# Optimization experiments

Measured on AMD Instinct MI355X. Metric: run time of the kernel, lower is better.

Reference implementation:

```python
import jax, jax.numpy as jnp
import numpy as np

B, S, D, H = 4, 2048, 1024, 16
DK = D // H
INFTY = 1000000.0
INIT_SCALE = 1.2  # RandomUniform(-1.2, 1.2) kernel initializer


def setup_inputs() -> dict:
    key = jax.random.key(0)
    ks = jax.random.split(key, 6)
    x = jax.random.normal(ks[0], (B, S, D), dtype=jnp.float32)
    mask = jax.random.randint(ks[1], (B, S), 0, 2) == 1  # bool padding mask
    WQ = jax.random.uniform(ks[2], (D, D), jnp.float32, -INIT_SCALE, INIT_SCALE)
    WK = jax.random.uniform(ks[3], (D, D), jnp.float32, -INIT_SCALE, INIT_SCALE)
    WV = jax.random.uniform(ks[4], (D, D), jnp.float32, -INIT_SCALE, INIT_SCALE)
    WO = jax.random.uniform(ks[5], (D, D), jnp.float32, -INIT_SCALE, INIT_SCALE)
    return {"x": x, "mask": mask, "WQ": WQ, "WK": WK, "WV": WV, "WO": WO}


def reference(x, mask, WQ, WK, WV, WO):
    # Faithful reproduction of the layout: reshape to (B, S, d_key, n_heads)
    # then permute, matching K.reshape/K.permute_dimensions in the original.
    q = (x @ WQ).reshape(B, S, DK, H).transpose(0, 3, 1, 2)  # (B, H, S, DK)
    k = (x @ WK).reshape(B, S, DK, H).transpose(0, 3, 2, 1)  # (B, H, DK, S)
    score = jnp.matmul(q, k) / np.sqrt(DK)                   # (B, H, S, S)
    # additive key masking: score - (~mask)[B,1,1,S] * infinity
    inv_mask = (~mask).astype(x.dtype)
    score = score - inv_mask[:, None, None, :] * INFTY
    score = jax.nn.softmax(score, axis=-1)                   # att_dropout == 0
    v = (x @ WV).reshape(B, S, DK, H).transpose(0, 3, 1, 2)  # (B, H, S, DK)
    o = jnp.matmul(score, v)                                 # (B, H, S, DK)
    o = o.transpose(0, 2, 1, 3).reshape(B, S, H * DK)
    o = o @ WO                                               # (B, S, D)
    # final query-position masking + abs, as in the original
    o = jnp.abs(o * mask.astype(x.dtype)[:, :, None])
    return o
```

## Files before the change

### kernel.cpp

```cpp
#include <hip/hip_runtime.h>
#include <hip/hip_bf16.h>
#include <cstdint>
#include <cstddef>

constexpr int Bc  = 4;
constexpr int Sc  = 2048;
constexpr int Dc  = 1024;
constexpr int Hc  = 16;
constexpr int DKc = 64;
constexpr int Mtot = Bc * Sc;
constexpr float SC2  = 0.125f * 1.4426950408889634f;
constexpr float INF2 = 1000000.0f * 1.4426950408889634f;
constexpr float SXq  = 5400.0f;
constexpr float SWq  = 27166.0f;
constexpr float INVS = 1.0f / (SXq * SWq);

typedef short bf16x8 __attribute__((ext_vector_type(8)));
typedef float f32x4  __attribute__((ext_vector_type(4)));
typedef int   i32x4  __attribute__((ext_vector_type(4)));
typedef unsigned int u32x4 __attribute__((ext_vector_type(4)));

__device__ inline unsigned short bf16_rn(float f) {
    uint32_t u = __float_as_uint(f);
    uint32_t r = (u + 0x7FFFu + ((u >> 16) & 1u)) >> 16;
    return (unsigned short)r;
}
__device__ inline uint32_t pk_bf16(float a, float b) {
    uint32_t d;
    asm("v_cvt_pk_bf16_f32 %0, %1, %2" : "=v"(d) : "v"(a), "v"(b));
    return d;
}
__device__ inline int perm64(int k) {
    return (k & ~63) | (((k & 15) << 2) | ((k >> 4) & 3));
}
__device__ inline void mfma_i8(i32x4& acc, u32x4 a, u32x4 b) {
    asm volatile("v_mfma_i32_16x16x64_i8 %0, %1, %2, %0" : "+v"(acc) : "v"(a), "v"(b));
}
__device__ inline void split_i16(int fx, char& h, char& l) {
    int lo = ((fx + 128) & 255) - 128;
    h = (char)((fx - lo) >> 8);
    l = (char)lo;
}
__device__ inline void gl_lds16(const void* g, void* l) {
    __builtin_amdgcn_global_load_lds(
        (const __attribute__((address_space(1))) unsigned int*)g,
        (__attribute__((address_space(3))) unsigned int*)l, 16, 0, 0);
}

__global__ __launch_bounds__(256) void mask_norm(const void* __restrict__ mraw,
                                                 int* __restrict__ mi,
                                                 int* __restrict__ rinv,
                                                 int* __restrict__ nbv,
                                                 int* __restrict__ npadv) {
    __shared__ int fF32, fU8, fI32;
    __shared__ int part[256];
    __shared__ int nb_sh;
    if (threadIdx.x == 0) { fF32 = 0; fU8 = 0; fI32 = 0; }
    __syncthreads();
    const unsigned char* mb = (const unsigned char*)mraw;
    int aF = 0, a1 = 0, a4 = 0;
    for (int i = threadIdx.x; i < Mtot; i += 256) {
        unsigned char v = mb[i];
        if ((i & 3) == 3 && v == 0x3F) aF = 1;
        if (v) {
            if (i & 3) a1 = 1;
            else if (i & 7) a4 = 1;
        }
    }
    if (aF) fF32 = 1;
    if (a1) fU8 = 1;
    if (a4) fI32 = 1;
    __syncthreads();
    if (fF32) {
        const float* mf = (const float*)mraw;
        for (int s = threadIdx.x; s < Mtot; s += 256) mi[s] = (mf[s] != 0.0f);
    } else if (fU8) {
        for (int s = threadIdx.x; s < Mtot; s += 256) mi[s] = (mb[s] != 0);
    } else if (fI32) {
        const int* m32 = (const int*)mraw;
        for (int s = threadIdx.x; s < Mtot; s += 256) mi[s] = (m32[s] != 0);
    } else {
        const long long* m64 = (const long long*)mraw;
        for (int s = threadIdx.x; s < Mtot; s += 256) mi[s] = (m64[s] != 0);
    }
    __syncthreads();

    for (int b = 0; b < Bc; ++b) {
        const int* mrow = mi + b * Sc;
        int loc[8], cnt = 0;
        #pragma unroll
        for (int u = 0; u < 8; ++u) {
            loc[u] = mrow[threadIdx.x * 8 + u];
            cnt += loc[u];
        }
        part[threadIdx.x] = cnt;
        __syncthreads();
        if (threadIdx.x == 0) {
            int run = 0;
            for (int i = 0; i < 256; ++i) { int c = part[i]; part[i] = run; run += c; }
            nbv[b] = run;
            npadv[b] = (run + 63) & ~63;
            nb_sh = run;
        }
        __syncthreads();
        const int nbb = nb_sh;
        int pos = part[threadIdx.x];
        #pragma unroll
        for (int u = 0; u < 8; ++u) {
            const int s = threadIdx.x * 8 + u;
            if (loc[u]) {
                rinv[b * Sc + pos] = s;
                pos++;
            } else {
                rinv[b * Sc + nbb + (s - pos)] = s;
            }
        }
        __syncthreads();
    }
}

__global__ __launch_bounds__(256) void zero_pad(const int* __restrict__ nbv,
                                                const int* __restrict__ npadv,
                                                unsigned short* __restrict__ Khi,
                                                unsigned short* __restrict__ Klo,
                                                unsigned short* __restrict__ Vt) {
    const int bh = blockIdx.x;
    const int b = bh >> 4;
    const int nb = nbv[b], np = npadv[b];
    const int t = threadIdx.x;
    const size_t kbase = (size_t)bh * Sc * DKc;
    const size_t vbase = (size_t)bh * DKc * Sc;
    const int n = (np - nb) * DKc;
    for (int i = t; i < n; i += 256) {
        const int r = nb + i / DKc, c = i % DKc;
        Khi[kbase + (size_t)r * DKc + c] = 0;
        Klo[kbase + (size_t)r * DKc + c] = 0;
        Vt[vbase + (size_t)c * Sc + r] = 0;
    }
}

__global__ __launch_bounds__(256) void quant_x(const float* __restrict__ x,
                                               unsigned short* __restrict__ xhi,
                                               signed char* __restrict__ xh8,
                                               signed char* __restrict__ xl8) {
    const int i = (blockIdx.x * 256 + threadIdx.x) * 4;
    float4 v = *reinterpret_cast<const float4*>(x + i);
    ushort4 hb;
    hb.x = bf16_rn(v.x); hb.y = bf16_rn(v.y); hb.z = bf16_rn(v.z); hb.w = bf16_rn(v.w);
    *reinterpret_cast<ushort4*>(xhi + i) = hb;
    char4 h8, l8;
    int fx;
    fx = min(max(__float2int_rn(v.x * SXq), -32640), 32640); split_i16(fx, h8.x, l8.x);
    fx = min(max(__float2int_rn(v.y * SXq), -32640), 32640); split_i16(fx, h8.y, l8.y);
    fx = min(max(__float2int_rn(v.z * SXq), -32640), 32640); split_i16(fx, h8.z, l8.z);
    fx = min(max(__float2int_rn(v.w * SXq), -32640), 32640); split_i16(fx, h8.w, l8.w);
    *reinterpret_cast<char4*>(xh8 + i) = h8;
    *reinterpret_cast<char4*>(xl8 + i) = l8;
}

template<bool PERM>
__global__ __launch_bounds__(256) void split_wt(const float* __restrict__ W,
                                                unsigned short* __restrict__ WhT) {
    __shared__ float ls[64][68];
    const int k0 = blockIdx.y * 64, n0 = blockIdx.x * 64;
    const int t = threadIdx.x;
    #pragma unroll
    for (int l = 0; l < 4; ++l) {
        const int idx = t + l * 256;
        const int r = idx >> 4, c = (idx & 15) * 4;
        *reinterpret_cast<float4*>(&ls[r][c]) =
            *reinterpret_cast<const float4*>(W + (size_t)(k0 + r) * Dc + n0 + c);
    }
    __syncthreads();
    #pragma unroll
    for (int l = 0; l < 4; ++l) {
        const int idx = t + l * 256;
        const int on = idx >> 4, kq = (idx & 15) * 4;
        #pragma unroll
        for (int j = 0; j < 4; ++j) {
            const float v = ls[kq + j][on];
            const int k  = k0 + kq + j;
            const int kd = PERM ? perm64(k) : k;
            WhT[(size_t)(n0 + on) * Dc + kd] = bf16_rn(v);
        }
    }
}

__global__ __launch_bounds__(256) void split_wt_i8(const float* __restrict__ W,
                                                   signed char* __restrict__ Wh8,
                                                   signed char* __restrict__ Wl8) {
    __shared__ float ls[64][68];
    const int k0 = blockIdx.y * 64, n0 = blockIdx.x * 64;
    const int t = threadIdx.x;
    #pragma unroll
    for (int l = 0; l < 4; ++l) {
        const int idx = t + l * 256;
        const int r = idx >> 4, c = (idx & 15) * 4;
        *reinterpret_cast<float4*>(&ls[r][c]) =
            *reinterpret_cast<const float4*>(W + (size_t)(k0 + r) * Dc + n0 + c);
    }
    __syncthreads();
    #pragma unroll
    for (int l = 0; l < 4; ++l) {
        const int idx = t + l * 256;
        const int on = idx >> 4, kq = (idx & 15) * 4;
        char4 hv, lv;
        int fx;
        fx = __float2int_rn(ls[kq + 0][on] * SWq); split_i16(fx, hv.x, lv.x);
        fx = __float2int_rn(ls[kq + 1][on] * SWq); split_i16(fx, hv.y, lv.y);
        fx = __float2int_rn(ls[kq + 2][on] * SWq); split_i16(fx, hv.z, lv.z);
        fx = __float2int_rn(ls[kq + 3][on] * SWq); split_i16(fx, hv.w, lv.w);
        const size_t o = (size_t)(n0 + on) * Dc + k0 + kq;
        *reinterpret_cast<char4*>(Wh8 + o) = hv;
        *reinterpret_cast<char4*>(Wl8 + o) = lv;
    }
}

__global__ __launch_bounds__(256) void gemm_i8qk(
    const signed char* __restrict__ Ah8, const signed char* __restrict__ Al8,
    const signed char* __restrict__ Bh8, const signed char* __restrict__ Bl8,
    const int* __restrict__ rinv, const int* __restrict__ nbv, float scale,
    unsigned short* __restrict__ O1, unsigned short* __restrict__ O2) {
    __shared__ __align__(16) signed char Ah[128 * 64];
    __shared__ __align__(16) signed char Al[128 * 64];
    __shared__ __align__(16) signed char Bh[128 * 64];
    __shared__ __align__(16) signed char Bl[128 * 64];
    const int t = threadIdx.x;
    const int n0 = blockIdx.x * 128, m0 = blockIdx.y * 128;
    const int b = m0 >> 11, mm0 = m0 & 2047;
    const int nb = nbv[b];
    if (mm0 >= nb) return;
    const int wv = t >> 6, lane = t & 63, li = lane & 15, lg = lane >> 4;
    const int wm = (wv >> 1) * 64, wn = (wv & 1) * 64;

    size_t gAr[2];
    int rowN[2];
    #pragma unroll
    for (int c = 0; c < 2; ++c) {
        const int ci  = wv * 2 + c;
        const int row = ci * 16 + (lane >> 2);
        rowN[c] = n0 + row;
        gAr[c] = ((size_t)b * Sc + rinv[b * Sc + mm0 + row]) * Dc;
    }
    const int cq = (lane & 3) * 16;

    i32x4 a1[4][4] = {};
    i32x4 a2[4][4] = {};
    asm volatile("s_nop 7" :::);

    for (int k0 = 0; k0 < Dc; k0 += 64) {
        __syncthreads();
        #pragma unroll
        for (int c = 0; c < 2; ++c) {
            const int ci = wv * 2 + c;
            const size_t ga = gAr[c] + k0 + cq;
            const size_t gb = (size_t)rowN[c] * Dc + k0 + cq;
            gl_lds16(Ah8 + ga, &Ah[ci * 1024]);
            gl_lds16(Al8 + ga, &Al[ci * 1024]);
            gl_lds16(Bh8 + gb, &Bh[ci * 1024]);
            gl_lds16(Bl8 + gb, &Bl[ci * 1024]);
        }
        __syncthreads();

        u32x4 bhf[4], blf[4];
        #pragma unroll
        for (int ni = 0; ni < 4; ++ni) {
            bhf[ni] = *reinterpret_cast<const u32x4*>(&Bh[(wn + ni * 16 + li) * 64 + lg * 16]);
            blf[ni] = *reinterpret_cast<const u32x4*>(&Bl[(wn + ni * 16 + li) * 64 + lg * 16]);
        }
        #pragma unroll
        for (int mi = 0; mi < 4; ++mi) {
            const u32x4 ahf = *reinterpret_cast<const u32x4*>(&Ah[(wm + mi * 16 + li) * 64 + lg * 16]);
            const u32x4 alf = *reinterpret_cast<const u32x4*>(&Al[(wm + mi * 16 + li) * 64 + lg * 16]);
            #pragma unroll
            for (int ni = 0; ni < 4; ++ni) {
                mfma_i8(a1[mi][ni], ahf, bhf[ni]);
                mfma_i8(a2[mi][ni], ahf, blf[ni]);
                mfma_i8(a2[mi][ni], alf, bhf[ni]);
            }
        }
    }

    asm volatile("s_nop 7\ns_nop 7\ns_nop 7" :::);

    const int dkb = (n0 + wn) >> 4;
    #pragma unroll
    for (int mi = 0; mi < 4; ++mi) {
        #pragma unroll
        for (int r = 0; r < 4; ++r) {
            const int cs = mm0 + wm + mi * 16 + lg * 4 + r;
            if (cs >= nb) continue;
            const size_t ob = ((size_t)(b * Hc + li) * Sc + cs) * DKc + dkb;
            ushort4 hq, lq;
            float fv[4];
            #pragma unroll
            for (int ni = 0; ni < 4; ++ni)
                fv[ni] = fmaf((float)a1[mi][ni][r], 65536.0f,
                              (float)a2[mi][ni][r] * 256.0f) * scale;
            hq.x = bf16_rn(fv[0]); hq.y = bf16_rn(fv[1]);
            hq.z = bf16_rn(fv[2]); hq.w = bf16_rn(fv[3]);
            lq.x = bf16_rn(fv[0] - __uint_as_float((uint32_t)hq.x << 16));
            lq.y = bf16_rn(fv[1] - __uint_as_float((uint32_t)hq.y << 16));
            lq.z = bf16_rn(fv[2] - __uint_as_float((uint32_t)hq.z << 16));
            lq.w = bf16_rn(fv[3] - __uint_as_float((uint32_t)hq.w << 16));
            *reinterpret_cast<ushort4*>(O1 + ob) = hq;
            *reinterpret_cast<ushort4*>(O2 + ob) = lq;
        }
    }
}

template<int EPI>
__global__ __launch_bounds__(256) void gemm_bf16(
    const unsigned short* __restrict__ Ahi,
    const unsigned short* __restrict__ Bhi,
    const int* __restrict__ rinv, const int* __restrict__ nbv,
    unsigned short* __restrict__ O1,
    float* __restrict__ Of) {
    __shared__ __align__(16) unsigned short Ah[128 * 32];
    __shared__ __align__(16) unsigned short Bh[128 * 32];
    const int t = threadIdx.x;
    const int n0 = blockIdx.x * 128, m0 = blockIdx.y * 128;
    const int b = m0 >> 11, mm0 = m0 & 2047;
    const int nb = nbv[b];
    const int wv = t >> 6, lane = t & 63, li = lane & 15, lg = lane >> 4;
    const int wm = (wv >> 1) * 64, wn = (wv & 1) * 64;

    if (EPI == 1 && mm0 >= nb) return;
    if (EPI == 2 && mm0 >= nb) {
        #pragma unroll
        for (int mi = 0; mi < 4; ++mi) {
            #pragma unroll
            for (int r = 0; r < 4; ++r) {
                const int cs = mm0 + wm + mi * 16 + lg * 4 + r;
                const int gs = rinv[b * Sc + cs];
                #pragma unroll
                for (int ni = 0; ni < 4; ++ni) {
                    const int n = n0 + wn + ni * 16 + li;
                    Of[((size_t)(b * Sc + gs)) * Dc + n] = 0.0f;
                }
            }
        }
        return;
    }

    size_t gAr[2];
    int rowN[2];
    #pragma unroll
    for (int c = 0; c < 2; ++c) {
        const int ci  = wv * 2 + c;
        const int row = ci * 16 + (lane >> 2);
        rowN[c] = n0 + row;
        if (EPI == 1)
            gAr[c] = ((size_t)b * Sc + rinv[b * Sc + mm0 + row]) * Dc;
        else
            gAr[c] = (size_t)(m0 + row) * Dc;
    }
    const int cq = (lane & 3) * 8;

    f32x4 acc[4][4] = {};

    for (int k0 = 0; k0 < Dc; k0 += 32) {
        __syncthreads();
        #pragma unroll
        for (int c = 0; c < 2; ++c) {
            const int ci = wv * 2 + c;
            gl_lds16(Ahi + gAr[c] + k0 + cq, &Ah[ci * 512]);
            gl_lds16(Bhi + (size_t)rowN[c] * Dc + k0 + cq, &Bh[ci * 512]);
        }
        __syncthreads();

        bf16x8 bhf[4];
        #pragma unroll
        for (int ni = 0; ni < 4; ++ni)
            bhf[ni] = *reinterpret_cast<const bf16x8*>(&Bh[(wn + ni * 16 + li) * 32 + lg * 8]);
        #pragma unroll
        for (int mi = 0; mi < 4; ++mi) {
            const bf16x8 ahf = *reinterpret_cast<const bf16x8*>(&Ah[(wm + mi * 16 + li) * 32 + lg * 8]);
            #pragma unroll
            for (int ni = 0; ni < 4; ++ni)
                acc[mi][ni] = __builtin_amdgcn_mfma_f32_16x16x32_bf16(ahf, bhf[ni], acc[mi][ni], 0, 0, 0);
        }
    }

    #pragma unroll
    for (int mi = 0; mi < 4; ++mi) {
        if (EPI == 1) {
            const int csb = mm0 + wm + mi * 16 + lg * 4;
            #pragma unroll
            for (int ni = 0; ni < 4; ++ni) {
                const int n = n0 + wn + ni * 16 + li;
                const int h = n & 15, dk = n >> 4;
                const size_t ob = ((size_t)(b * Hc + h) * DKc + dk) * Sc + csb;
                if (csb + 3 < nb) {
                    ushort4 vq;
                    vq.x = bf16_rn(acc[mi][ni][0]);
                    vq.y = bf16_rn(acc[mi][ni][1]);
                    vq.z = bf16_rn(acc[mi][ni][2]);
                    vq.w = bf16_rn(acc[mi][ni][3]);
                    *reinterpret_cast<ushort4*>(O1 + ob) = vq;
                } else {
                    #pragma unroll
                    for (int r = 0; r < 4; ++r)
                        if (csb + r < nb) O1[ob + r] = bf16_rn(acc[mi][ni][r]);
                }
            }
        } else {
            #pragma unroll
            for (int r = 0; r < 4; ++r) {
                const int cs = mm0 + wm + mi * 16 + lg * 4 + r;
                const int gs = rinv[b * Sc + cs];
                const bool valid = (cs < nb);
                #pragma unroll
                for (int ni = 0; ni < 4; ++ni) {
                    const int n = n0 + wn + ni * 16 + li;
                    Of[((size_t)(b * Sc + gs)) * Dc + n] =
                        valid ? fabsf(acc[mi][ni][r]) : 0.0f;
                }
            }
        }
    }
}

__global__ __launch_bounds__(512) void attn_mfma(const unsigned short* __restrict__ Qhi,
                                                 const unsigned short* __restrict__ Qlo,
                                                 const unsigned short* __restrict__ Khi,
                                                 const unsigned short* __restrict__ Klo,
                                                 const unsigned short* __restrict__ Vtg,
                                                 const int* __restrict__ nbv,
                                                 const int* __restrict__ npadv,
                                                 unsigned short* __restrict__ att) {
    constexpr int TK = 64;
    const int id  = blockIdx.x;
    const int swz = (id & 7) * 128 + (id >> 3);
    const int qb  = swz & 15;
    const int bh  = swz >> 4;
    const int b = bh >> 4, h = bh & 15;
    const int q0 = qb * 128;
    const int nb = nbv[b];
    if (q0 >= nb) return;
    const int ntile = npadv[b] >> 6;
    const int nt2 = (ntile + 1) >> 1;

    __shared__ __align__(16) unsigned short PsKs[2][128][72];
    __shared__ __align__(16) unsigned short Vs[2][80][72];

    const int t    = threadIdx.x;
    const int grp  = t >> 8;
    const int tg   = t & 255;
    const int wave = tg >> 6;
    const int lane = t & 63;
    const int lg   = lane >> 4;
    const int li   = lane & 15;

    const int myBase = grp ? nt2 : 0;
    const int myEnd  = grp ? ntile : nt2;

    {
        const int r = 64 + (tg >> 4), c4 = (tg & 15) * 4;
        const unsigned short val = ((tg >> 4) == 0) ? (unsigned short)0x3F80 : (unsigned short)0;
        ushort4 v; v.x = val; v.y = val; v.z = val; v.w = val;
        *reinterpret_cast<ushort4*>(&Vs[grp][r][c4]) = v;
    }

    bf16x8 qh[2][2], ql[2][2];
    #pragma unroll
    for (int hf = 0; hf < 2; ++hf) {
        const size_t qrow = ((size_t)bh * Sc + q0 + wave * 32 + hf * 16 + li) * DKc + lg * 8;
        qh[hf][0] = *reinterpret_cast<const bf16x8*>(Qhi + qrow);
        qh[hf][1] = *reinterpret_cast<const bf16x8*>(Qhi + qrow + 32);
        ql[hf][0] = *reinterpret_cast<const bf16x8*>(Qlo + qrow);
        ql[hf][1] = *reinterpret_cast<const bf16x8*>(Qlo + qrow + 32);
    }

    const size_t kbase = (size_t)bh * Sc * DKc;
    const size_t vbase = (size_t)bh * DKc * Sc;

    f32x4 accO[2][5] = {};
    float m[2][4];
    #pragma unroll
    for (int hf = 0; hf < 2; ++hf)
        #pragma unroll
        for (int r = 0; r < 4; ++r) m[hf][r] = -1e30f;

    for (int it = 0; it < nt2; ++it) {
        const int kt = myBase + it;
        const bool act = (kt < myEnd);
        const int k0 = kt * TK;
        __syncthreads();
        if (act) {
            #pragma unroll
            for (int u = 0; u < 2; ++u) {
                const int idx = tg + u * 256;
                const int r = idx >> 3, cc = (idx & 7) * 8;
                *reinterpret_cast<uint4*>(&PsKs[grp][r][cc]) =
                    *reinterpret_cast<const uint4*>(Khi + kbase + (size_t)(k0 + r) * DKc + cc);
                *reinterpret_cast<uint4*>(&PsKs[grp][64 + r][cc]) =
                    *reinterpret_cast<const uint4*>(Klo + kbase + (size_t)(k0 + r) * DKc + cc);
                *reinterpret_cast<uint4*>(&Vs[grp][r][cc]) =
                    *reinterpret_cast<const uint4*>(Vtg + vbase + (size_t)r * Sc + k0 + cc);
            }
        }
        __syncthreads();
        if (!act) continue;

        float sc[2][4][4];
        #pragma unroll
        for (int n = 0; n < 4; ++n) {
            const bf16x8 kh0 = *reinterpret_cast<const bf16x8*>(&PsKs[grp][n * 16 + li][lg * 8]);
            const bf16x8 kh1 = *reinterpret_cast<const bf16x8*>(&PsKs[grp][n * 16 + li][32 + lg * 8]);
            const bf16x8 kl0 = *reinterpret_cast<const bf16x8*>(&PsKs[grp][64 + n * 16 + li][lg * 8]);
            const bf16x8 kl1 = *reinterpret_cast<const bf16x8*>(&PsKs[grp][64 + n * 16 + li][32 + lg * 8]);
            const float mz = (k0 + n * 16 + li < nb) ? 0.0f : INF2;
            #pragma unroll
            for (int hf = 0; hf < 2; ++hf) {
                f32x4 a = {0, 0, 0, 0};
                a = __builtin_amdgcn_mfma_f32_16x16x32_bf16(qh[hf][0], kh0, a, 0, 0, 0);
                a = __builtin_amdgcn_mfma_f32_16x16x32_bf16(qh[hf][1], kh1, a, 0, 0, 0);
                a = __builtin_amdgcn_mfma_f32_16x16x32_bf16(qh[hf][0], kl0, a, 0, 0, 0);
                a = __builtin_amdgcn_mfma_f32_16x16x32_bf16(qh[hf][1], kl1, a, 0, 0, 0);
                a = __builtin_amdgcn_mfma_f32_16x16x32_bf16(ql[hf][0], kh0, a, 0, 0, 0);
                a = __builtin_amdgcn_mfma_f32_16x16x32_bf16(ql[hf][1], kh1, a, 0, 0, 0);
                #pragma unroll
                for (int r = 0; r < 4; ++r) sc[hf][n][r] = a[r] - mz;
            }
        }

        float mx[2][4], rs[2][4];
        #pragma unroll
        for (int hf = 0; hf < 2; ++hf)
            #pragma unroll
            for (int r = 0; r < 4; ++r)
                mx[hf][r] = fmaxf(fmaxf(sc[hf][0][r], sc[hf][1][r]),
                                  fmaxf(sc[hf][2][r], sc[hf][3][r]));
        #pragma unroll
        for (int o = 1; o < 16; o <<= 1)
            #pragma unroll
            for (int hf = 0; hf < 2; ++hf)
                #pragma unroll
                for (int r = 0; r < 4; ++r)
                    mx[hf][r] = fmaxf(mx[hf][r], __shfl_xor(mx[hf][r], o));
        #pragma unroll
        for (int hf = 0; hf < 2; ++hf)
            #pragma unroll
            for (int r = 0; r < 4; ++r) {
                const float mn = fmaxf(m[hf][r], mx[hf][r]);
                rs[hf][r] = exp2f(m[hf][r] - mn);
                m[hf][r]  = mn;
            }
        #pragma unroll
        for (int hf = 0; hf < 2; ++hf)
            #pragma unroll
            for (int r = 0; r < 4; ++r) {
                const int row = wave * 32 + hf * 16 + lg * 4 + r;
                const uint32_t w01 = pk_bf16(exp2f(sc[hf][0][r] - m[hf][r]),
                                             exp2f(sc[hf][1][r] - m[hf][r]));
                const uint32_t w23 = pk_bf16(exp2f(sc[hf][2][r] - m[hf][r]),
                                             exp2f(sc[hf][3][r] - m[hf][r]));
                PsKs[grp][row][li]      = (unsigned short)w01;
                PsKs[grp][row][li + 16] = (unsigned short)(w01 >> 16);
                PsKs[grp][row][li + 32] = (unsigned short)w23;
                PsKs[grp][row][li + 48] = (unsigned short)(w23 >> 16);
            }

        #pragma unroll
        for (int hf = 0; hf < 2; ++hf)
            #pragma unroll
            for (int dt = 0; dt < 5; ++dt)
                #pragma unroll
                for (int r = 0; r < 4; ++r)
                    accO[hf][dt][r] *= rs[hf][r];

        #pragma unroll
        for (int c = 0; c < 2; ++c) {
            bf16x8 pa[2];
            #pragma unroll
            for (int hf = 0; hf < 2; ++hf)
                pa[hf] = *reinterpret_cast<const bf16x8*>(&PsKs[grp][wave * 32 + hf * 16 + li][c * 32 + lg * 8]);
            #pragma unroll
            for (int dt = 0; dt < 5; ++dt) {
                const bf16x8 vb = *reinterpret_cast<const bf16x8*>(&Vs[grp][dt * 16 + li][c * 32 + lg * 8]);
                #pragma unroll
                for (int hf = 0; hf < 2; ++hf)
                    accO[hf][dt] = __builtin_amdgcn_mfma_f32_16x16x32_bf16(pa[hf], vb, accO[hf][dt], 0, 0, 0);
            }
        }
    }

    __syncthreads();
    float* pO  = (float*)&PsKs[0][0][0];
    float* pML = pO + 128 * 64;

    if (grp == 1) {
        #pragma unroll
        for (int hf = 0; hf < 2; ++hf) {
            #pragma unroll
            for (int r = 0; r < 4; ++r) {
                const int row = wave * 32 + hf * 16 + lg * 4 + r;
                if (li == 0) {
                    pML[row * 2]     = m[hf][r];
                    pML[row * 2 + 1] = accO[hf][4][r];
                }
                float4 o = make_float4(accO[hf][0][r], accO[hf][1][r],
                                       accO[hf][2][r], accO[hf][3][r]);
                *reinterpret_cast<float4*>(&pO[row * 64 + li * 4]) = o;
            }
        }
    }
    __syncthreads();
    if (grp == 0) {
        #pragma unroll
        for (int hf = 0; hf < 2; ++hf) {
            #pragma unroll
            for (int r = 0; r < 4; ++r) {
                const int row = wave * 32 + hf * 16 + lg * 4 + r;
                const float m1 = pML[row * 2];
                const float l1 = pML[row * 2 + 1];
                const float l0 = __shfl(accO[hf][4][r], lane & 0x30);
                const float ms = fmaxf(m[hf][r], m1);
                const float s0 = exp2f(m[hf][r] - ms);
                const float s1 = exp2f(m1 - ms);
                const float inv = 1.0f / (l0 * s0 + l1 * s1);
                const float4 o1 = *reinterpret_cast<const float4*>(&pO[row * 64 + li * 4]);
                const int q = q0 + row;
                uint2 w;
                w.x = pk_bf16((accO[hf][0][r] * s0 + o1.x * s1) * inv,
                              (accO[hf][1][r] * s0 + o1.y * s1) * inv);
                w.y = pk_bf16((accO[hf][2][r] * s0 + o1.z * s1) * inv,
                              (accO[hf][3][r] * s0 + o1.w * s1) * inv);
                *reinterpret_cast<uint2*>(att + (size_t)(b * Sc + q) * Dc + h * DKc + li * 4) = w;
            }
        }
    }
}

extern "C" void kernel_launch(void* const* d_in, const int* in_sizes, int n_in,
                              void* d_out, int out_size, void* d_ws, size_t ws_size,
                              hipStream_t stream) {
    const float* x    = (const float*)d_in[0];
    const void*  mraw = d_in[1];
    const float* WQ   = (const float*)d_in[2];
    const float* WK   = (const float*)d_in[3];
    const float* WV   = (const float*)d_in[4];
    const float* WO   = (const float*)d_in[5];
    float* out = (float*)d_out;

    int* mi    = (int*)d_ws;
    int* rinv  = mi + Mtot;
    int* nbv   = rinv + Mtot;
    int* npadv = nbv + 4;
    const size_t SZ = (size_t)Mtot * Dc;
    const size_t WSZ = (size_t)Dc * Dc;
    char* p = (char*)d_ws + 65664;
    unsigned short* xhi = (unsigned short*)p;            p += SZ * 2;
    signed char*    xh8 = (signed char*)p;               p += SZ;
    signed char*    xl8 = (signed char*)p;               p += SZ;
    unsigned short* WVh = (unsigned short*)p;            p += WSZ * 2;
    unsigned short* WOh = (unsigned short*)p;            p += WSZ * 2;
    signed char*    WQh8 = (signed char*)p;              p += WSZ;
    signed char*    WQl8 = (signed char*)p;              p += WSZ;
    signed char*    WKh8 = (signed char*)p;              p += WSZ;
    signed char*    WKl8 = (signed char*)p;              p += WSZ;
    unsigned short* Qhi = (unsigned short*)p;            p += SZ * 2;
    unsigned short* Qlo = (unsigned short*)p;            p += SZ * 2;
    unsigned short* Khi = (unsigned short*)p;            p += SZ * 2;
    unsigned short* Klo = (unsigned short*)p;            p += SZ * 2;
    unsigned short* Vt  = (unsigned short*)p;            p += SZ * 2;
    unsigned short* att = xhi;

    mask_norm<<<1, 256, 0, stream>>>(mraw, mi, rinv, nbv, npadv);
    quant_x<<<(int)(SZ / 1024), 256, 0, stream>>>(x, xhi, xh8, xl8);
    const dim3 gW(16, 16);
    split_wt_i8<<<gW, 256, 0, stream>>>(WQ, WQh8, WQl8);
    split_wt_i8<<<gW, 256, 0, stream>>>(WK, WKh8, WKl8);
    split_wt<false><<<gW, 256, 0, stream>>>(WV, WVh);
    split_wt<true ><<<gW, 256, 0, stream>>>(WO, WOh);
    zero_pad<<<dim3(64), 256, 0, stream>>>(nbv, npadv, Khi, Klo, Vt);

    const dim3 gG(Dc / 128, Mtot / 128);
    gemm_i8qk<<<gG, 256, 0, stream>>>(xh8, xl8, WQh8, WQl8, rinv, nbv, SC2 * INVS, Qhi, Qlo);
    gemm_i8qk<<<gG, 256, 0, stream>>>(xh8, xl8, WKh8, WKl8, rinv, nbv, INVS, Khi, Klo);
    gemm_bf16<1><<<gG, 256, 0, stream>>>(xhi, WVh, rinv, nbv, Vt, nullptr);

    attn_mfma<<<dim3(1024), 512, 0, stream>>>(Qhi, Qlo, Khi, Klo, Vt, nbv, npadv, att);

    gemm_bf16<2><<<gG, 256, 0, stream>>>(att, WOh, rinv, nbv, nullptr, out);
}
```

Baseline: 298.8 us.

## Merge prep kernels and QKV GEMMs into batched launches, parallelize mask per batch

```diff
diff --git a/kernel.cpp b/kernel.cpp
--- a/kernel.cpp
+++ b/kernel.cpp
@@ -48,7 +48,6 @@
 }
 
 __global__ __launch_bounds__(256) void mask_norm(const void* __restrict__ mraw,
-                                                 int* __restrict__ mi,
                                                  int* __restrict__ rinv,
                                                  int* __restrict__ nbv,
                                                  int* __restrict__ npadv) {
@@ -71,71 +70,47 @@
     if (a1) fU8 = 1;
     if (a4) fI32 = 1;
     __syncthreads();
+
+    const int b = blockIdx.x;
+    const int sbase = b * Sc + threadIdx.x * 8;
+    int loc[8], cnt = 0;
     if (fF32) {
         const float* mf = (const float*)mraw;
-        for (int s = threadIdx.x; s < Mtot; s += 256) mi[s] = (mf[s] != 0.0f);
+        #pragma unroll
+        for (int u = 0; u < 8; ++u) { loc[u] = (mf[sbase + u] != 0.0f); cnt += loc[u]; }
     } else if (fU8) {
-        for (int s = threadIdx.x; s < Mtot; s += 256) mi[s] = (mb[s] != 0);
+        #pragma unroll
+        for (int u = 0; u < 8; ++u) { loc[u] = (mb[sbase + u] != 0); cnt += loc[u]; }
     } else if (fI32) {
         const int* m32 = (const int*)mraw;
-        for (int s = threadIdx.x; s < Mtot; s += 256) mi[s] = (m32[s] != 0);
+        #pragma unroll
+        for (int u = 0; u < 8; ++u) { loc[u] = (m32[sbase + u] != 0); cnt += loc[u]; }
     } else {
         const long long* m64 = (const long long*)mraw;
-        for (int s = threadIdx.x; s < Mtot; s += 256) mi[s] = (m64[s] != 0);
-    }
+        #pragma unroll
+        for (int u = 0; u < 8; ++u) { loc[u] = (m64[sbase + u] != 0); cnt += loc[u]; }
+    }
+    part[threadIdx.x] = cnt;
     __syncthreads();
-
-    for (int b = 0; b < Bc; ++b) {
-        const int* mrow = mi + b * Sc;
-        int loc[8], cnt = 0;
-        #pragma unroll
-        for (int u = 0; u < 8; ++u) {
-            loc[u] = mrow[threadIdx.x * 8 + u];
-            cnt += loc[u];
-        }
-        part[threadIdx.x] = cnt;
-        __syncthreads();
-        if (threadIdx.x == 0) {
-            int run = 0;
-            for (int i = 0; i < 256; ++i) { int c = part[i]; part[i] = run; run += c; }
-            nbv[b] = run;
-            npadv[b] = (run + 63) & ~63;
-            nb_sh = run;
-        }
-        __syncthreads();
-        const int nbb = nb_sh;
-        int pos = part[threadIdx.x];
-        #pragma unroll
-        for (int u = 0; u < 8; ++u) {
-            const int s = threadIdx.x * 8 + u;
-            if (loc[u]) {
-                rinv[b * Sc + pos] = s;
-                pos++;
-            } else {
-                rinv[b * Sc + nbb + (s - pos)] = s;
-            }
-        }
-        __syncthreads();
-    }
-}
-
-__global__ __launch_bounds__(256) void zero_pad(const int* __restrict__ nbv,
-                                                const int* __restrict__ npadv,
-                                                unsigned short* __restrict__ Khi,
-                                                unsigned short* __restrict__ Klo,
-                                                unsigned short* __restrict__ Vt) {
-    const int bh = blockIdx.x;
-    const int b = bh >> 4;
-    const int nb = nbv[b], np = npadv[b];
-    const int t = threadIdx.x;
-    const size_t kbase = (size_t)bh * Sc * DKc;
-    const size_t vbase = (size_t)bh * DKc * Sc;
-    const int n = (np - nb) * DKc;
-    for (int i = t; i < n; i += 256) {
-        const int r = nb + i / DKc, c = i % DKc;
-        Khi[kbase + (size_t)r * DKc + c] = 0;
-        Klo[kbase + (size_t)r * DKc + c] = 0;
-        Vt[vbase + (size_t)c * Sc + r] = 0;
+    if (threadIdx.x == 0) {
+        int run = 0;
+        for (int i = 0; i < 256; ++i) { int c = part[i]; part[i] = run; run += c; }
+        nbv[b] = run;
+        npadv[b] = (run + 63) & ~63;
+        nb_sh = run;
+    }
+    __syncthreads();
+    const int nbb = nb_sh;
+    int pos = part[threadIdx.x];
+    #pragma unroll
+    for (int u = 0; u < 8; ++u) {
+        const int s = threadIdx.x * 8 + u;
+        if (loc[u]) {
+            rinv[b * Sc + pos] = s;
+            pos++;
+        } else {
+            rinv[b * Sc + nbb + (s - pos)] = s;
+        }
     }
 }
 
@@ -158,12 +133,38 @@
     *reinterpret_cast<char4*>(xl8 + i) = l8;
 }
 
-template<bool PERM>
-__global__ __launch_bounds__(256) void split_wt(const float* __restrict__ W,
-                                                unsigned short* __restrict__ WhT) {
+__global__ __launch_bounds__(256) void prep_w(
+    const float* __restrict__ WQ, const float* __restrict__ WK,
+    const float* __restrict__ WV, const float* __restrict__ WO,
+    signed char* __restrict__ WQh8, signed char* __restrict__ WQl8,
+    signed char* __restrict__ WKh8, signed char* __restrict__ WKl8,
+    unsigned short* __restrict__ WVh, unsigned short* __restrict__ WOh,
+    const int* __restrict__ nbv, const int* __restrict__ npadv,
+    unsigned short* __restrict__ Khi, unsigned short* __restrict__ Klo,
+    unsigned short* __restrict__ Vt) {
+    const int z = blockIdx.z;
+    const int t = threadIdx.x;
+
+    if (z == 4) {
+        const int idx = blockIdx.y * 16 + blockIdx.x;
+        const int bh = idx >> 2, prt = idx & 3;
+        const int b = bh >> 4;
+        const int nb = nbv[b], np = npadv[b];
+        const size_t kbase = (size_t)bh * Sc * DKc;
+        const size_t vbase = (size_t)bh * DKc * Sc;
+        const int n = (np - nb) * DKc;
+        for (int i = prt * 256 + t; i < n; i += 1024) {
+            const int r = nb + i / DKc, c = i % DKc;
+            Khi[kbase + (size_t)r * DKc + c] = 0;
+            Klo[kbase + (size_t)r * DKc + c] = 0;
+            Vt[vbase + (size_t)c * Sc + r] = 0;
+        }
+        return;
+    }
+
     __shared__ float ls[64][68];
+    const float* W = (z == 0) ? WQ : (z == 1) ? WK : (z == 2) ? WV : WO;
     const int k0 = blockIdx.y * 64, n0 = blockIdx.x * 64;
-    const int t = threadIdx.x;
     #pragma unroll
     for (int l = 0; l < 4; ++l) {
         const int idx = t + l * 256;
@@ -172,59 +173,54 @@
             *reinterpret_cast<const float4*>(W + (size_t)(k0 + r) * Dc + n0 + c);
     }
     __syncthreads();
-    #pragma unroll
-    for (int l = 0; l < 4; ++l) {
-        const int idx = t + l * 256;
-        const int on = idx >> 4, kq = (idx & 15) * 4;
-        #pragma unroll
-        for (int j = 0; j < 4; ++j) {
-            const float v = ls[kq + j][on];
-            const int k  = k0 + kq + j;
-            const int kd = PERM ? perm64(k) : k;
-            WhT[(size_t)(n0 + on) * Dc + kd] = bf16_rn(v);
-        }
-    }
-}
-
-__global__ __launch_bounds__(256) void split_wt_i8(const float* __restrict__ W,
-                                                   signed char* __restrict__ Wh8,
-                                                   signed char* __restrict__ Wl8) {
-    __shared__ float ls[64][68];
-    const int k0 = blockIdx.y * 64, n0 = blockIdx.x * 64;
-    const int t = threadIdx.x;
-    #pragma unroll
-    for (int l = 0; l < 4; ++l) {
-        const int idx = t + l * 256;
-        const int r = idx >> 4, c = (idx & 15) * 4;
-        *reinterpret_cast<float4*>(&ls[r][c]) =
-            *reinterpret_cast<const float4*>(W + (size_t)(k0 + r) * Dc + n0 + c);
-    }
-    __syncthreads();
-    #pragma unroll
-    for (int l = 0; l < 4; ++l) {
-        const int idx = t + l * 256;
-        const int on = idx >> 4, kq = (idx & 15) * 4;
-        char4 hv, lv;
-        int fx;
-        fx = __float2int_rn(ls[kq + 0][on] * SWq); split_i16(fx, hv.x, lv.x);
-        fx = __float2int_rn(ls[kq + 1][on] * SWq); split_i16(fx, hv.y, lv.y);
-        fx = __float2int_rn(ls[kq + 2][on] * SWq); split_i16(fx, hv.z, lv.z);
-        fx = __float2int_rn(ls[kq + 3][on] * SWq); split_i16(fx, hv.w, lv.w);
-        const size_t o = (size_t)(n0 + on) * Dc + k0 + kq;
-        *reinterpret_cast<char4*>(Wh8 + o) = hv;
-        *reinterpret_cast<char4*>(Wl8 + o) = lv;
-    }
-}
-
-__global__ __launch_bounds__(256) void gemm_i8qk(
-    const signed char* __restrict__ Ah8, const signed char* __restrict__ Al8,
-    const signed char* __restrict__ Bh8, const signed char* __restrict__ Bl8,
-    const int* __restrict__ rinv, const int* __restrict__ nbv, float scale,
-    unsigned short* __restrict__ O1, unsigned short* __restrict__ O2) {
-    __shared__ __align__(16) signed char Ah[128 * 64];
-    __shared__ __align__(16) signed char Al[128 * 64];
-    __shared__ __align__(16) signed char Bh[128 * 64];
-    __shared__ __align__(16) signed char Bl[128 * 64];
+
+    if (z <= 1) {
+        signed char* Wh8 = z ? WKh8 : WQh8;
+        signed char* Wl8 = z ? WKl8 : WQl8;
+        #pragma unroll
+        for (int l = 0; l < 4; ++l) {
+            const int idx = t + l * 256;
+            const int on = idx >> 4, kq = (idx & 15) * 4;
+            char4 hv, lv;
+            int fx;
+            fx = __float2int_rn(ls[kq + 0][on] * SWq); split_i16(fx, hv.x, lv.x);
+            fx = __float2int_rn(ls[kq + 1][on] * SWq); split_i16(fx, hv.y, lv.y);
+            fx = __float2int_rn(ls[kq + 2][on] * SWq); split_i16(fx, hv.z, lv.z);
+            fx = __float2int_rn(ls[kq + 3][on] * SWq); split_i16(fx, hv.w, lv.w);
+            const size_t o = (size_t)(n0 + on) * Dc + k0 + kq;
+            *reinterpret_cast<char4*>(Wh8 + o) = hv;
+            *reinterpret_cast<char4*>(Wl8 + o) = lv;
+        }
+    } else {
+        unsigned short* Wh = (z == 2) ? WVh : WOh;
+        const bool PERM = (z == 3);
+        #pragma unroll
+        for (int l = 0; l < 4; ++l) {
+            const int idx = t + l * 256;
+            const int on = idx >> 4, kq = (idx & 15) * 4;
+            #pragma unroll
+            for (int j = 0; j < 4; ++j) {
+                const float v = ls[kq + j][on];
+                const int k  = k0 + kq + j;
+                const int kd = PERM ? perm64(k) : k;
+                Wh[(size_t)(n0 + on) * Dc + kd] = bf16_rn(v);
+            }
+        }
+    }
+}
+
+__global__ __launch_bounds__(256) void gemm_qkv(
+    const signed char* __restrict__ xh8, const signed char* __restrict__ xl8,
+    const unsigned short* __restrict__ xhi,
+    const signed char* __restrict__ WQh8, const signed char* __restrict__ WQl8,
+    const signed char* __restrict__ WKh8, const signed char* __restrict__ WKl8,
+    const unsigned short* __restrict__ WVh,
+    const int* __restrict__ rinv, const int* __restrict__ nbv,
+    unsigned short* __restrict__ Qhi, unsigned short* __restrict__ Qlo,
+    unsigned short* __restrict__ Khi, unsigned short* __restrict__ Klo,
+    unsigned short* __restrict__ Vt) {
+    __shared__ __align__(16) char S[32768];
+    const int z = blockIdx.z;
     const int t = threadIdx.x;
     const int n0 = blockIdx.x * 128, m0 = blockIdx.y * 128;
     const int b = m0 >> 11, mm0 = m0 & 2047;
@@ -233,158 +229,133 @@
     const int wv = t >> 6, lane = t & 63, li = lane & 15, lg = lane >> 4;
     const int wm = (wv >> 1) * 64, wn = (wv & 1) * 64;
 
-    size_t gAr[2];
-    int rowN[2];
-    #pragma unroll
-    for (int c = 0; c < 2; ++c) {
-        const int ci  = wv * 2 + c;
-        const int row = ci * 16 + (lane >> 2);
-        rowN[c] = n0 + row;
-        gAr[c] = ((size_t)b * Sc + rinv[b * Sc + mm0 + row]) * Dc;
-    }
-    const int cq = (lane & 3) * 16;
-
-    i32x4 a1[4][4] = {};
-    i32x4 a2[4][4] = {};
-    asm volatile("s_nop 7" :::);
-
-    for (int k0 = 0; k0 < Dc; k0 += 64) {
-        __syncthreads();
+    if (z < 2) {
+        signed char* Ah = (signed char*)S;
+        signed char* Al = (signed char*)S + 8192;
+        signed char* Bh = (signed char*)S + 16384;
+        signed char* Bl = (signed char*)S + 24576;
+        const signed char* Bh8 = z ? WKh8 : WQh8;
+        const signed char* Bl8 = z ? WKl8 : WQl8;
+        const float scale = z ? INVS : (SC2 * INVS);
+        unsigned short* O1 = z ? Khi : Qhi;
+        unsigned short* O2 = z ? Klo : Qlo;
+
+        size_t gAr[2];
+        int rowN[2];
         #pragma unroll
         for (int c = 0; c < 2; ++c) {
-            const int ci = wv * 2 + c;
-            const size_t ga = gAr[c] + k0 + cq;
-            const size_t gb = (size_t)rowN[c] * Dc + k0 + cq;
-            gl_lds16(Ah8 + ga, &Ah[ci * 1024]);
-            gl_lds16(Al8 + ga, &Al[ci * 1024]);
-            gl_lds16(Bh8 + gb, &Bh[ci * 1024]);
-            gl_lds16(Bl8 + gb, &Bl[ci * 1024]);
-        }
-        __syncthreads();
-
-        u32x4 bhf[4], blf[4];
-        #pragma unroll
-        for (int ni = 0; ni < 4; ++ni) {
-            bhf[ni] = *reinterpret_cast<const u32x4*>(&Bh[(wn + ni * 16 + li) * 64 + lg * 16]);
-            blf[ni] = *reinterpret_cast<const u32x4*>(&Bl[(wn + ni * 16 + li) * 64 + lg * 16]);
-        }
-        #pragma unroll
-        for (int mi = 0; mi < 4; ++mi) {
-            const u32x4 ahf = *reinterpret_cast<const u32x4*>(&Ah[(wm + mi * 16 + li) * 64 + lg * 16]);
-            const u32x4 alf = *reinterpret_cast<const u32x4*>(&Al[(wm + mi * 16 + li) * 64 + lg * 16]);
+            const int ci  = wv * 2 + c;
+            const int row = ci * 16 + (lane >> 2);
+            rowN[c] = n0 + row;
+            gAr[c] = ((size_t)b * Sc + rinv[b * Sc + mm0 + row]) * Dc;
+        }
+        const int cq = (lane & 3) * 16;
+
+        i32x4 a1[4][4] = {};
+        i32x4 a2[4][4] = {};
+        asm volatile("s_nop 7" :::);
+
+        for (int k0 = 0; k0 < Dc; k0 += 64) {
+            __syncthreads();
+            #pragma unroll
+            for (int c = 0; c < 2; ++c) {
+                const int ci = wv * 2 + c;
+                const size_t ga = gAr[c] + k0 + cq;
+                const size_t gb = (size_t)rowN[c] * Dc + k0 + cq;
+                gl_lds16(xh8 + ga, &Ah[ci * 1024]);
+                gl_lds16(xl8 + ga, &Al[ci * 1024]);
+                gl_lds16(Bh8 + gb, &Bh[ci * 1024]);
+                gl_lds16(Bl8 + gb, &Bl[ci * 1024]);
+            }
+            __syncthreads();
+
+            u32x4 bhf[4], blf[4];
             #pragma unroll
             for (int ni = 0; ni < 4; ++ni) {
-                mfma_i8(a1[mi][ni], ahf, bhf[ni]);
-                mfma_i8(a2[mi][ni], ahf, blf[ni]);
-                mfma_i8(a2[mi][ni], alf, bhf[ni]);
-            }
-        }
-    }
-
-    asm volatile("s_nop 7\ns_nop 7\ns_nop 7" :::);
-
-    const int dkb = (n0 + wn) >> 4;
-    #pragma unroll
-    for (int mi = 0; mi < 4; ++mi) {
-        #pragma unroll
-        for (int r = 0; r < 4; ++r) {
-            const int cs = mm0 + wm + mi * 16 + lg * 4 + r;
-            if (cs >= nb) continue;
-            const size_t ob = ((size_t)(b * Hc + li) * Sc + cs) * DKc + dkb;
-            ushort4 hq, lq;
-            float fv[4];
-            #pragma unroll
-            for (int ni = 0; ni < 4; ++ni)
-                fv[ni] = fmaf((float)a1[mi][ni][r], 65536.0f,
-                              (float)a2[mi][ni][r] * 256.0f) * scale;
-            hq.x = bf16_rn(fv[0]); hq.y = bf16_rn(fv[1]);
-            hq.z = bf16_rn(fv[2]); hq.w = bf16_rn(fv[3]);
-            lq.x = bf16_rn(fv[0] - __uint_as_float((uint32_t)hq.x << 16));
-            lq.y = bf16_rn(fv[1] - __uint_as_float((uint32_t)hq.y << 16));
-            lq.z = bf16_rn(fv[2] - __uint_as_float((uint32_t)hq.z << 16));
-            lq.w = bf16_rn(fv[3] - __uint_as_float((uint32_t)hq.w << 16));
-            *reinterpret_cast<ushort4*>(O1 + ob) = hq;
-            *reinterpret_cast<ushort4*>(O2 + ob) = lq;
-        }
-    }
-}
-
-template<int EPI>
-__global__ __launch_bounds__(256) void gemm_bf16(
-    const unsigned short* __restrict__ Ahi,
-    const unsigned short* __restrict__ Bhi,
-    const int* __restrict__ rinv, const int* __restrict__ nbv,
-    unsigned short* __restrict__ O1,
-    float* __restrict__ Of) {
-    __shared__ __align__(16) unsigned short Ah[128 * 32];
-    __shared__ __align__(16) unsigned short Bh[128 * 32];
-    const int t = threadIdx.x;
-    const int n0 = blockIdx.x * 128, m0 = blockIdx.y * 128;
-    const int b = m0 >> 11, mm0 = m0 & 2047;
-    const int nb = nbv[b];
-    const int wv = t >> 6, lane = t & 63, li = lane & 15, lg = lane >> 4;
-    const int wm = (wv >> 1) * 64, wn = (wv & 1) * 64;
-
-    if (EPI == 1 && mm0 >= nb) return;
-    if (EPI == 2 && mm0 >= nb) {
+                bhf[ni] = *reinterpret_cast<const u32x4*>(&Bh[(wn + ni * 16 + li) * 64 + lg * 16]);
+                blf[ni] = *reinterpret_cast<const u32x4*>(&Bl[(wn + ni * 16 + li) * 64 + lg * 16]);
+            }
+            #pragma unroll
+            for (int mi = 0; mi < 4; ++mi) {
+                const u32x4 ahf = *reinterpret_cast<const u32x4*>(&Ah[(wm + mi * 16 + li) * 64 + lg * 16]);
+                const u32x4 alf = *reinterpret_cast<const u32x4*>(&Al[(wm + mi * 16 + li) * 64 + lg * 16]);
+                #pragma unroll
+                for (int ni = 0; ni < 4; ++ni) {
+                    mfma_i8(a1[mi][ni], ahf, bhf[ni]);
+                    mfma_i8(a2[mi][ni], ahf, blf[ni]);
+                    mfma_i8(a2[mi][ni], alf, bhf[ni]);
+                }
+            }
+        }
+
+        asm volatile("s_nop 7\ns_nop 7\ns_nop 7" :::);
+
+        const int dkb = (n0 + wn) >> 4;
         #pragma unroll
         for (int mi = 0; mi < 4; ++mi) {
             #pragma unroll
             for (int r = 0; r < 4; ++r) {
                 const int cs = mm0 + wm + mi * 16 + lg * 4 + r;
-                const int gs = rinv[b * Sc + cs];
+                if (cs >= nb) continue;
+                const size_t ob = ((size_t)(b * Hc + li) * Sc + cs) * DKc + dkb;
+                ushort4 hq, lq;
+                float fv[4];
                 #pragma unroll
-                for (int ni = 0; ni < 4; ++ni) {
-                    const int n = n0 + wn + ni * 16 + li;
-                    Of[((size_t)(b * Sc + gs)) * Dc + n] = 0.0f;
-                }
-            }
-        }
-        return;
-    }
-
-    size_t gAr[2];
-    int rowN[2];
-    #pragma unroll
-    for (int c = 0; c < 2; ++c) {
-        const int ci  = wv * 2 + c;
-        const int row = ci * 16 + (lane >> 2);
-        rowN[c] = n0 + row;
-        if (EPI == 1)
+                for (int ni = 0; ni < 4; ++ni)
+                    fv[ni] = fmaf((float)a1[mi][ni][r], 65536.0f,
+                                  (float)a2[mi][ni][r] * 256.0f) * scale;
+                hq.x = bf16_rn(fv[0]); hq.y = bf16_rn(fv[1]);
+                hq.z = bf16_rn(fv[2]); hq.w = bf16_rn(fv[3]);
+                lq.x = bf16_rn(fv[0] - __uint_as_float((uint32_t)hq.x << 16));
+                lq.y = bf16_rn(fv[1] - __uint_as_float((uint32_t)hq.y << 16));
+                lq.z = bf16_rn(fv[2] - __uint_as_float((uint32_t)hq.z << 16));
+                lq.w = bf16_rn(fv[3] - __uint_as_float((uint32_t)hq.w << 16));
+                *reinterpret_cast<ushort4*>(O1 + ob) = hq;
+                *reinterpret_cast<ushort4*>(O2 + ob) = lq;
+            }
+        }
+    } else {
+        unsigned short* Ah = (unsigned short*)S;
+        unsigned short* Bh = (unsigned short*)(S + 8192);
+
+        size_t gAr[2];
+        int rowN[2];
+        #pragma unroll
+        for (int c = 0; c < 2; ++c) {
+            const int ci  = wv * 2 + c;
+            const int row = ci * 16 + (lane >> 2);
+            rowN[c] = n0 + row;
             gAr[c] = ((size_t)b * Sc + rinv[b * Sc + mm0 + row]) * Dc;
-        else
-            gAr[c] = (size_t)(m0 + row) * Dc;
-    }
-    const int cq = (lane & 3) * 8;
-
-    f32x4 acc[4][4] = {};
-
-    for (int k0 = 0; k0 < Dc; k0 += 32) {
-        __syncthreads();
-        #pragma unroll
-        for (int c = 0; c < 2; ++c) {
-            const int ci = wv * 2 + c;
-            gl_lds16(Ahi + gAr[c] + k0 + cq, &Ah[ci * 512]);
-            gl_lds16(Bhi + (size_t)rowN[c] * Dc + k0 + cq, &Bh[ci * 512]);
-        }
-        __syncthreads();
-
-        bf16x8 bhf[4];
-        #pragma unroll
-        for (int ni = 0; ni < 4; ++ni)
-            bhf[ni] = *reinterpret_cast<const bf16x8*>(&Bh[(wn + ni * 16 + li) * 32 + lg * 8]);
+        }
+        const int cq = (lane & 3) * 8;
+
+        f32x4 acc[4][4] = {};
+
+        for (int k0 = 0; k0 < Dc; k0 += 32) {
+            __syncthreads();
+            #pragma unroll
+            for (int c = 0; c < 2; ++c) {
+                const int ci = wv * 2 + c;
+                gl_lds16(xhi + gAr[c] + k0 + cq, &Ah[ci * 512]);
+                gl_lds16(WVh + (size_t)rowN[c] * Dc + k0 + cq, &Bh[ci * 512]);
+            }
+            __syncthreads();
+
+            bf16x8 bhf[4];
+            #pragma unroll
+            for (int ni = 0; ni < 4; ++ni)
+                bhf[ni] = *reinterpret_cast<const bf16x8*>(&Bh[(wn + ni * 16 + li) * 32 + lg * 8]);
+            #pragma unroll
+            for (int mi = 0; mi < 4; ++mi) {
+                const bf16x8 ahf = *reinterpret_cast<const bf16x8*>(&Ah[(wm + mi * 16 + li) * 32 + lg * 8]);
+                #pragma unroll
+                for (int ni = 0; ni < 4; ++ni)
+                    acc[mi][ni] = __builtin_amdgcn_mfma_f32_16x16x32_bf16(ahf, bhf[ni], acc[mi][ni], 0, 0, 0);
+            }
+        }
+
         #pragma unroll
         for (int mi = 0; mi < 4; ++mi) {
-            const bf16x8 ahf = *reinterpret_cast<const bf16x8*>(&Ah[(wm + mi * 16 + li) * 32 + lg * 8]);
-            #pragma unroll
-            for (int ni = 0; ni < 4; ++ni)
-                acc[mi][ni] = __builtin_amdgcn_mfma_f32_16x16x32_bf16(ahf, bhf[ni], acc[mi][ni], 0, 0, 0);
-        }
-    }
-
-    #pragma unroll
-    for (int mi = 0; mi < 4; ++mi) {
-        if (EPI == 1) {
             const int csb = mm0 + wm + mi * 16 + lg * 4;
             #pragma unroll
             for (int ni = 0; ni < 4; ++ni) {
@@ -397,25 +368,87 @@
                     vq.y = bf16_rn(acc[mi][ni][1]);
                     vq.z = bf16_rn(acc[mi][ni][2]);
                     vq.w = bf16_rn(acc[mi][ni][3]);
-                    *reinterpret_cast<ushort4*>(O1 + ob) = vq;
+                    *reinterpret_cast<ushort4*>(Vt + ob) = vq;
                 } else {
                     #pragma unroll
                     for (int r = 0; r < 4; ++r)
-                        if (csb + r < nb) O1[ob + r] = bf16_rn(acc[mi][ni][r]);
+                        if (csb + r < nb) Vt[ob + r] = bf16_rn(acc[mi][ni][r]);
                 }
             }
-        } else {
+        }
+    }
+}
+
+__global__ __launch_bounds__(256) void gemm_oproj(
+    const unsigned short* __restrict__ Ahi,
+    const unsigned short* __restrict__ Bhi,
+    const int* __restrict__ rinv, const int* __restrict__ nbv,
+    float* __restrict__ Of) {
+    __shared__ __align__(16) unsigned short Ah[128 * 32];
+    __shared__ __align__(16) unsigned short Bh[128 * 32];
+    const int t = threadIdx.x;
+    const int n0 = blockIdx.x * 128, m0 = blockIdx.y * 128;
+    const int b = m0 >> 11, mm0 = m0 & 2047;
+    const int nb = nbv[b];
+    const int wv = t >> 6, lane = t & 63, li = lane & 15, lg = lane >> 4;
+    const int wm = (wv >> 1) * 64, wn = (wv & 1) * 64;
+
+    if (mm0 >= nb) {
+        #pragma unroll
+        for (int mi = 0; mi < 4; ++mi) {
             #pragma unroll
             for (int r = 0; r < 4; ++r) {
                 const int cs = mm0 + wm + mi * 16 + lg * 4 + r;
                 const int gs = rinv[b * Sc + cs];
-                const bool valid = (cs < nb);
                 #pragma unroll
                 for (int ni = 0; ni < 4; ++ni) {
                     const int n = n0 + wn + ni * 16 + li;
-                    Of[((size_t)(b * Sc + gs)) * Dc + n] =
-                        valid ? fabsf(acc[mi][ni][r]) : 0.0f;
+                    Of[((size_t)(b * Sc + gs)) * Dc + n] = 0.0f;
                 }
+            }
+        }
+        return;
+    }
+
+    f32x4 acc[4][4] = {};
+
+    for (int k0 = 0; k0 < Dc; k0 += 32) {
+        __syncthreads();
+        #pragma unroll
+        for (int c = 0; c < 2; ++c) {
+            const int ci  = wv * 2 + c;
+            const int row = ci * 16 + (lane >> 2);
+            const int cq  = (lane & 3) * 8;
+            gl_lds16(Ahi + (size_t)(m0 + row) * Dc + k0 + cq, &Ah[ci * 512]);
+            gl_lds16(Bhi + (size_t)(n0 + row) * Dc + k0 + cq, &Bh[ci * 512]);
+        }
+        __syncthreads();
+
+        bf16x8 bhf[4];
+        #pragma unroll
+        for (int ni = 0; ni < 4; ++ni)
+            bhf[ni] = *reinterpret_cast<const bf16x8*>(&Bh[(wn + ni * 16 + li) * 32 + lg * 8]);
+        #pragma unroll
+        for (int mi = 0; mi < 4; ++mi) {
+            const bf16x8 ahf = *reinterpret_cast<const bf16x8*>(&Ah[(wm + mi * 16 + li) * 32 + lg * 8]);
+            #pragma unroll
+            for (int ni = 0; ni < 4; ++ni)
+                acc[mi][ni] = __builtin_amdgcn_mfma_f32_16x16x32_bf16(ahf, bhf[ni], acc[mi][ni], 0, 0, 0);
+        }
+    }
+
+    #pragma unroll
+    for (int mi = 0; mi < 4; ++mi) {
+        #pragma unroll
+        for (int r = 0; r < 4; ++r) {
+            const int cs = mm0 + wm + mi * 16 + lg * 4 + r;
+            const int gs = rinv[b * Sc + cs];
+            const bool valid = (cs < nb);
+            #pragma unroll
+            for (int ni = 0; ni < 4; ++ni) {
+                const int n = n0 + wn + ni * 16 + li;
+                Of[((size_t)(b * Sc + gs)) * Dc + n] =
+                    valid ? fabsf(acc[mi][ni][r]) : 0.0f;
             }
         }
     }
@@ -644,8 +677,7 @@
     const float* WO   = (const float*)d_in[5];
     float* out = (float*)d_out;
 
-    int* mi    = (int*)d_ws;
-    int* rinv  = mi + Mtot;
+    int* rinv  = (int*)d_ws;
     int* nbv   = rinv + Mtot;
     int* npadv = nbv + 4;
     const size_t SZ = (size_t)Mtot * Dc;
@@ -667,21 +699,19 @@
     unsigned short* Vt  = (unsigned short*)p;            p += SZ * 2;
     unsigned short* att = xhi;
 
-    mask_norm<<<1, 256, 0, stream>>>(mraw, mi, rinv, nbv, npadv);
+    mask_norm<<<dim3(4), 256, 0, stream>>>(mraw, rinv, nbv, npadv);
     quant_x<<<(int)(SZ / 1024), 256, 0, stream>>>(x, xhi, xh8, xl8);
-    const dim3 gW(16, 16);
-    split_wt_i8<<<gW, 256, 0, stream>>>(WQ, WQh8, WQl8);
-    split_wt_i8<<<gW, 256, 0, stream>>>(WK, WKh8, WKl8);
-    split_wt<false><<<gW, 256, 0, stream>>>(WV, WVh);
-    split_wt<true ><<<gW, 256, 0, stream>>>(WO, WOh);
-    zero_pad<<<dim3(64), 256, 0, stream>>>(nbv, npadv, Khi, Klo, Vt);
-
-    const dim3 gG(Dc / 128, Mtot / 128);
-    gemm_i8qk<<<gG, 256, 0, stream>>>(xh8, xl8, WQh8, WQl8, rinv, nbv, SC2 * INVS, Qhi, Qlo);
-    gemm_i8qk<<<gG, 256, 0, stream>>>(xh8, xl8, WKh8, WKl8, rinv, nbv, INVS, Khi, Klo);
-    gemm_bf16<1><<<gG, 256, 0, stream>>>(xhi, WVh, rinv, nbv, Vt, nullptr);
+    prep_w<<<dim3(16, 16, 5), 256, 0, stream>>>(WQ, WK, WV, WO,
+                                                WQh8, WQl8, WKh8, WKl8,
+                                                WVh, WOh, nbv, npadv,
+                                                Khi, Klo, Vt);
+
+    gemm_qkv<<<dim3(8, 64, 3), 256, 0, stream>>>(xh8, xl8, xhi,
+                                                 WQh8, WQl8, WKh8, WKl8, WVh,
+                                                 rinv, nbv,
+                                                 Qhi, Qlo, Khi, Klo, Vt);
 
     attn_mfma<<<dim3(1024), 512, 0, stream>>>(Qhi, Qlo, Khi, Klo, Vt, nbv, npadv, att);
 
-    gemm_bf16<2><<<gG, 256, 0, stream>>>(att, WOh, rinv, nbv, nullptr, out);
-}
+    gemm_oproj<<<dim3(8, 64), 256, 0, stream>>>(att, WOh, rinv, nbv, out);
+}
```

After: 289.8 us. 3.0% less time.
